# Optimization experiments

Measured on AMD Instinct MI355X. Metric: run time of the kernel, lower is better.

The kernel has to match this reference:

```python
import jax, jax.numpy as jnp
import numpy as np
import math

INNER = 96
EPS = 1e-8  # torch CosineSimilarity eps


def _proj(x, W1, W2):
    # nn.Linear(C,C,bias=False) -> ReLU -> nn.Linear(C,inner,bias=False)
    return jax.nn.relu(x @ W1) @ W2


def _cos(a, b):
    # torch CosineSimilarity(dim=-1): dot / (max(||a||,eps)*max(||b||,eps))
    num = jnp.sum(a * b, axis=-1)
    na = jnp.maximum(jnp.linalg.norm(a, axis=-1), EPS)
    nb = jnp.maximum(jnp.linalg.norm(b, axis=-1), EPS)
    return num / (na * nb)


def setup_inputs() -> dict:
    key = jax.random.key(0)
    ks = jax.random.split(key, 8)
    B, C, H, W = 128, 768, 7, 7
    sc1 = 1.0 / math.sqrt(C)
    inp = {
        "features_a": jax.random.normal(ks[0], (B, C, H, W), jnp.float32),
        "features_b": jax.random.normal(ks[1], (B, C, H, W), jnp.float32),
        "Wq1": jax.random.normal(ks[2], (C, C), jnp.float32) * sc1,
        "Wq2": jax.random.normal(ks[3], (C, INNER), jnp.float32) * sc1,
        "Wk1": jax.random.normal(ks[4], (C, C), jnp.float32) * sc1,
        "Wk2": jax.random.normal(ks[5], (C, INNER), jnp.float32) * sc1,
        "Wv1": jax.random.normal(ks[6], (C, C), jnp.float32) * sc1,
        "Wv2": jax.random.normal(ks[7], (C, INNER), jnp.float32) * sc1,
    }
    return inp


def reference(features_a, features_b, Wq1, Wq2, Wk1, Wk2, Wv1, Wv2):
    B, C = features_a.shape[0], features_a.shape[1]
    # [B, C, H, W] -> [B, S, C]
    fa = features_a.reshape(B, C, -1).transpose(0, 2, 1)
    fb = features_b.reshape(features_b.shape[0], C, -1).transpose(0, 2, 1)

    qa, ka, va = _proj(fa, Wq1, Wq2), _proj(fa, Wk1, Wk2), _proj(fa, Wv1, Wv2)
    qb, kb, vb = _proj(fb, Wq1, Wq2), _proj(fb, Wk1, Wk2), _proj(fb, Wv1, Wv2)

    scale = 1.0 / math.sqrt(INNER)

    # query_b vs key_a: [Bb, Ba, Sq, Sk]
    scores_ba = jnp.einsum('bqe,ake->baqk', qb, ka) * scale
    probs_ba = jax.nn.softmax(scores_ba, axis=-1)
    aligned_a = jnp.einsum('baqk,ake->baqe', probs_ba, va)  # [Bb, Ba, S, inner]

    # query_a vs key_b: [Bb, Ba, Sq, Sk]
    scores_ab = jnp.einsum('aqe,bke->baqk', qa, kb) * scale
    probs_ab = jax.nn.softmax(scores_ab, axis=-1)
    aligned_b = jnp.einsum('baqk,bke->baqe', probs_ab, vb)  # [Bb, Ba, S, inner]

    sim = _cos(va[None, :, :, :], aligned_b) + _cos(vb[:, None, :, :], aligned_a)
    return sim.mean(-1)  # [Bb, Ba]
```

## Files before the change

kernel.cpp:

```cpp
#include <hip/hip_runtime.h>
#include <hip/hip_bf16.h>
#include <math.h>

typedef __attribute__((ext_vector_type(8))) short bf16x8;
typedef __attribute__((ext_vector_type(4))) float f32x4;
typedef __attribute__((ext_vector_type(2))) float f32x2;

#define MROWS 12544
#define CDIM 768
#define INNER 96
#define S49 49
#define NSIDE 6272
#define SCALE 0.10206207261596577f
#define SCALE_EXP2 ((float)(0.10206207261596577 * 1.4426950408889634))

__device__ __forceinline__ unsigned short f2bf(float f) {
  union { float f; unsigned u; } v; v.f = f;
  unsigned u = v.u;
  return (unsigned short)((u + 0x7fffu + ((u >> 16) & 1u)) >> 16);
}
__device__ __forceinline__ float bf2f(unsigned short h) {
  union { unsigned u; float f; } v; v.u = ((unsigned)h) << 16;
  return v.f;
}
__device__ __forceinline__ unsigned pack_bf16_rn(float a, float b) {
  union { float f; unsigned u; } ua, ub; ua.f = a; ub.f = b;
  return __builtin_amdgcn_perm(ub.u + 0x8000u, ua.u + 0x8000u, 0x07060302u);
}

__device__ __forceinline__ void gld16(const unsigned short* g, unsigned short* l) {
  __builtin_amdgcn_global_load_lds(
      (const __attribute__((address_space(1))) unsigned int*)(g),
      (__attribute__((address_space(3))) unsigned int*)(l), 16, 0, 0);
}

__global__ __launch_bounds__(256) void prep_all(
    const float* __restrict__ fa, const float* __restrict__ fb,
    const float* __restrict__ w10, const float* __restrict__ w11,
    const float* __restrict__ w12, const float* __restrict__ w20,
    const float* __restrict__ w21, const float* __restrict__ w22,
    unsigned short* __restrict__ X,
    unsigned short* __restrict__ W1T, unsigned short* __restrict__ W2T,
    unsigned short* __restrict__ VtKpad) {
  const int t = threadIdx.x;
  int id = blockIdx.x;
  if (id < 3072) {
    __shared__ float T[64][50];
    const int z = id / 1536; id -= z * 1536;
    const int ct = id % 12, img = id / 12;
    const float* feat = z ? fb : fa;
    const float* src = feat + (size_t)img * (CDIM * S49) + (size_t)ct * 64 * S49;
    for (int idx = t; idx < 64 * S49; idx += 256) {
      int cc = idx / S49, s = idx - cc * S49;
      T[cc][s] = src[cc * S49 + s];
    }
    __syncthreads();
    unsigned short* dst = X + (size_t)(z * 128 + img) * S49 * CDIM + ct * 64;
    for (int idx = t; idx < S49 * 64; idx += 256) {
      int s = idx >> 6, cc = idx & 63;
      dst[(size_t)s * CDIM + cc] = f2bf(T[cc][s]);
    }
  } else if (id < 5016) {
    __shared__ float T[32][33];
    id -= 3072;
    const float* src;
    unsigned short* dst;
    int C, ctile, rtile;
    if (id < 1728) {
      int wdx = id / 576, tid = id - wdx * 576;
      ctile = tid % 24; rtile = tid / 24;
      src = wdx == 0 ? w10 : (wdx == 1 ? w11 : w12);
      dst = W1T + (size_t)wdx * CDIM * CDIM;
      C = CDIM;
    } else {
      id -= 1728;
      int wdx = id / 72, tid = id - wdx * 72;
      ctile = tid % 3; rtile = tid / 3;
      src = wdx == 0 ? w20 : (wdx == 1 ? w21 : w22);
      dst = W2T + (size_t)wdx * INNER * CDIM;
      C = INNER;
    }
    const int c0 = ctile * 32, r0 = rtile * 32;
    for (int idx = t; idx < 1024; idx += 256) {
      int rr = idx >> 5, cc = idx & 31;
      T[rr][cc] = src[(size_t)(r0 + rr) * C + c0 + cc];
    }
    __syncthreads();
    for (int idx = t; idx < 1024; idx += 256) {
      int rr = idx >> 5, cc = idx & 31;
      dst[(size_t)(c0 + rr) * CDIM + r0 + cc] = f2bf(T[cc][rr]);
    }
  } else {
    id -= 5016;
    ushort4* p4 = (ushort4*)VtKpad;
    const ushort4 z = make_ushort4(0, 0, 0, 0);
#pragma unroll
    for (int i = 0; i < 32; i++)
      p4[(size_t)id * 8192 + i * 256 + t] = z;
  }
}

#define BARR() do { __builtin_amdgcn_sched_barrier(0); \
  __builtin_amdgcn_s_barrier(); __builtin_amdgcn_sched_barrier(0); } while (0)
#define STG(src, dhalf) do { \
  gld16((src), (dhalf) + t8); \
  gld16((src) + 32, (dhalf) + t8 + 4096); } while (0)
#define MFMA_QUAD(QM, QN) do { \
  __builtin_amdgcn_s_setprio(1); \
  _Pragma("unroll") \
  for (int mi = 0; mi < 4; ++mi) { \
    _Pragma("unroll") \
    for (int ni = 0; ni < 2; ++ni) { \
      _Pragma("unroll") \
      for (int ks = 0; ks < 2; ++ks) \
        acc[(QM)*4+mi][(QN)*2+ni] = __builtin_amdgcn_mfma_f32_16x16x32_bf16( \
            Af[mi*2+ks], Bf[((QN)*2+ni)*2+ks], acc[(QM)*4+mi][(QN)*2+ni], \
            0, 0, 0); \
    } \
  } \
  __builtin_amdgcn_s_setprio(0); } while (0)

__global__ __launch_bounds__(512, 2) void gemm1_8p(
    const unsigned short* __restrict__ X,
    const unsigned short* __restrict__ W1T,
    unsigned short* __restrict__ H, int wbase, int hsel) {
  __shared__ __align__(16) unsigned short L[2][4][8192];
  const int t = threadIdx.x;
  const int lane = t & 63, w = t >> 6;
  const int lr = lane & 15, lq = lane >> 4;
  const int wm2 = w >> 2, wn4 = w & 3;
  const int gx = gridDim.x, gxy = gx * gridDim.y;
  const int nwg = gxy * gridDim.z;
  const int orig = blockIdx.x + gx * (blockIdx.y + gridDim.y * blockIdx.z);
  const int q8 = nwg >> 3, r8 = nwg & 7;
  const int xcd = orig & 7, rank = orig >> 3;
  const int logical = (xcd < r8 ? xcd * (q8 + 1) : r8 * (q8 + 1) + (xcd - r8) * q8) + rank;
  const int wdx_l = logical / gxy;
  const int rem = logical - wdx_l * gxy;
  const int M0 = (rem / gx) * 256, N0 = (rem % gx) * 256;
  const int wdx = wdx_l + wbase;
  const unsigned short* W1w = W1T + (size_t)wdx * CDIM * CDIM;
  unsigned short* Hw = H + (hsel ? (size_t)wdx * MROWS * CDIM : 0);

  const int rs = t >> 2;
  const int cs = ((t & 3) * 8) ^ (((rs >> 3) & 1) << 4);
  const int soff = rs * CDIM + cs;
  const unsigned short* pA0 = X + (size_t)M0 * CDIM + soff;
  const unsigned short* pA1 = pA0 + (size_t)128 * CDIM;
  const unsigned short* pB0 = W1w + (size_t)N0 * CDIM + soff;
  const unsigned short* pB1 = pB0 + (size_t)128 * CDIM;
  const int t8 = t * 8;

  const int rdbase = lr * 32 + ((lq * 8) ^ (((lr >> 3) & 1) << 4));
  const int bO = (wn4 & 1) * 2048;

  const f32x4 z4 = {0.f, 0.f, 0.f, 0.f};
  f32x4 acc[8][4];
#pragma unroll
  for (int i = 0; i < 8; ++i)
#pragma unroll
    for (int j = 0; j < 4; ++j) acc[i][j] = z4;
  bf16x8 Af[8], Bf[8];

  STG(pB0, &L[0][2][0]);
  STG(pA0, &L[0][0][0]);
  STG(pA1, &L[0][1][0]);
  STG(pB1, &L[0][3][0]);
  STG(pB0 + 64, &L[1][2][0]);
  STG(pA0 + 64, &L[1][0][0]);
  asm volatile("s_waitcnt vmcnt(4)" ::: "memory");
  BARR();

  for (int tau = 0; tau < 12; ++tau) {
    const int buf = tau & 1;
    const unsigned short* LA = &L[buf][wm2][0];
    const unsigned short* LB = &L[buf][2 + (wn4 >> 1)][0];
#pragma unroll
    for (int mf = 0; mf < 4; ++mf)
#pragma unroll
      for (int ks = 0; ks < 2; ++ks)
        Af[mf * 2 + ks] = *(const bf16x8*)(LA + ks * 4096 + mf * 512 + rdbase);
#pragma unroll
    for (int nf = 0; nf < 2; ++nf)
#pragma unroll
      for (int ks = 0; ks < 2; ++ks)
        Bf[nf * 2 + ks] = *(const bf16x8*)(LB + ks * 4096 + bO + nf * 512 + rdbase);
    if (tau + 1 < 12) STG(pA1 + (tau + 1) * 64, &L[(tau + 1) & 1][1][0]);
    BARR();
    MFMA_QUAD(0, 0);
    BARR();
#pragma unroll
    for (int nf = 2; nf < 4; ++nf)
#pragma unroll
      for (int ks = 0; ks < 2; ++ks)
        Bf[nf * 2 + ks] = *(const bf16x8*)(LB + ks * 4096 + bO + nf * 512 + rdbase);
    if (tau + 1 < 12) STG(pB1 + (tau + 1) * 64, &L[(tau + 1) & 1][3][0]);
    BARR();
    MFMA_QUAD(0, 1);
    BARR();
#pragma unroll
    for (int mf = 4; mf < 8; ++mf)
#pragma unroll
      for (int ks = 0; ks < 2; ++ks)
        Af[(mf - 4) * 2 + ks] = *(const bf16x8*)(LA + ks * 4096 + mf * 512 + rdbase);
    if (tau + 2 < 12) STG(pB0 + (tau + 2) * 64, &L[buf][2][0]);
    BARR();
    MFMA_QUAD(1, 0);
    BARR();
    if (tau + 2 < 12) STG(pA0 + (tau + 2) * 64, &L[buf][0][0]);
    if (tau < 10) {
      asm volatile("s_waitcnt vmcnt(4)" ::: "memory");
    } else if (tau == 10) {
      asm volatile("s_waitcnt vmcnt(0)" ::: "memory");
    }
    BARR();
    MFMA_QUAD(1, 1);
    BARR();
  }
#pragma unroll
  for (int mf = 0; mf < 8; ++mf)
#pragma unroll
    for (int nf = 0; nf < 4; ++nf)
#pragma unroll
      for (int r = 0; r < 4; ++r) {
        int m = M0 + wm2 * 128 + mf * 16 + lq * 4 + r;
        int n = N0 + wn4 * 64 + nf * 16 + lr;
        Hw[(size_t)m * CDIM + n] = f2bf(fmaxf(acc[mf][nf][r], 0.f));
      }
}

__global__ __launch_bounds__(512) void gemm2b5(const unsigned short* __restrict__ H,
                                               const unsigned short* __restrict__ W2T,
                                               unsigned short* __restrict__ QKV,
                                               unsigned short* __restrict__ Kpad,
                                               unsigned short* __restrict__ Vt,
                                               float* __restrict__ vnorm,
                                               int wbase, int hsel) {
  __shared__ __align__(16) unsigned short As[64 * 128];
  __shared__ __align__(16) unsigned short Bs[96 * 128];
  const int t = threadIdx.x;
  const int lane = t & 63, w = t >> 6;
  const int lr = lane & 15, lq = lane >> 4;
  const int wm = w & 3, we = w >> 2;
  const int m0 = blockIdx.x * 64;
  const int wdx = blockIdx.y + wbase;
  const unsigned short* Hw = H + (hsel ? (size_t)wdx * MROWS * CDIM : 0);
  const unsigned short* W2w = W2T + (size_t)wdx * INNER * CDIM;
  const f32x4 z4 = {0.f, 0.f, 0.f, 0.f};
  f32x4 acc[3] = {z4, z4, z4};

  for (int k0 = 0; k0 < CDIM; k0 += 128) {
    __syncthreads();
#pragma unroll
    for (int j = 0; j < 2; j++) {
      int l = t + j * 512;
      int row = l >> 4, ch = l & 15;
      gld16(Hw + (size_t)(m0 + row) * CDIM + k0 + (ch ^ (row & 7)) * 8, As + l * 8);
    }
#pragma unroll
    for (int j = 0; j < 3; j++) {
      int l = t + j * 512;
      int row = l >> 4, ch = l & 15;
      gld16(W2w + (size_t)row * CDIM + k0 + (ch ^ (row & 7)) * 8, Bs + l * 8);
    }
    __syncthreads();
#pragma unroll
    for (int kk = 0; kk < 4; kk++) {
      int ca = (kk * 4 + lq) ^ (lr & 7);
      bf16x8 a = *(const bf16x8*)(As + (wm * 16 + lr) * 128 + ca * 8);
#pragma unroll
      for (int et = 0; et < 3; et++) {
        bf16x8 b = *(const bf16x8*)(Bs + (we * 48 + et * 16 + lr) * 128 + ca * 8);
        acc[et] = __builtin_amdgcn_mfma_f32_16x16x32_bf16(a, b, acc[et], 0, 0, 0);
      }
    }
  }
  float nsq[4] = {0.f, 0.f, 0.f, 0.f};
#pragma unroll
  for (int et = 0; et < 3; et++)
#pragma unroll
    for (int r = 0; r < 4; r++) {
      int m = m0 + wm * 16 + lq * 4 + r;
      int e = we * 48 + et * 16 + lr;
      float v = acc[et][r];
      int img = m / 49, s = m - img * 49;
      if (wdx == 0) {
        QKV[(size_t)m * INNER + e] = f2bf(v * SCALE_EXP2);
      } else if (wdx == 1) {
        Kpad[(size_t)(img * 64 + s) * INNER + e] = f2bf(v);
      } else {
        QKV[(size_t)(2 * MROWS + m) * INNER + e] = f2bf(v);
        Vt[(size_t)img * (INNER * 64) + e * 64 + s] = f2bf(v);
        nsq[r] += v * v;
      }
    }
  if (wdx == 2) {
    __syncthreads();
    float (*nsqp)[64] = (float (*)[64])As;
#pragma unroll
    for (int r = 0; r < 4; r++) {
      float p = nsq[r];
      p += __shfl_xor(p, 1, 16);
      p += __shfl_xor(p, 2, 16);
      p += __shfl_xor(p, 4, 16);
      p += __shfl_xor(p, 8, 16);
      if (lr == 0) nsqp[we][wm * 16 + lq * 4 + r] = p;
    }
    __syncthreads();
    if (t < 64) vnorm[m0 + t] = sqrtf(nsqp[0][t] + nsqp[1][t]);
  }
}

__global__ __launch_bounds__(256) void attn13(const unsigned short* __restrict__ Qp,
                                              const unsigned short* __restrict__ Kpad,
                                              const unsigned short* __restrict__ V,
                                              const unsigned short* __restrict__ Vt,
                                              const float* __restrict__ vnorm,
                                              float* __restrict__ cosbuf) {
  __shared__ __align__(16) unsigned short Ks[64 * INNER];
  __shared__ __align__(16) unsigned short VtS[INNER * 64];
  __shared__ __align__(16) unsigned short Ps[4][32 * 64];

  const int t = threadIdx.x;
  const int lane = t & 63, w = t >> 6;
  const int lr = lane & 15, lq = lane >> 4;
  const f32x4 z4 = {0.f, 0.f, 0.f, 0.f};

  int bx = blockIdx.x;
  const int dir = bx / 784; bx -= dir * 784;
  const int chunk = bx >> 4, fg = bx & 15;
  const int r0 = chunk * 128;
  const int qbase = dir * NSIDE;

  int goK[3], goV[3], lo[3];
#pragma unroll
  for (int j = 0; j < 3; j++) {
    int l = (w * 3 + j) * 64 + lane;
    lo[j] = l * 8;
    int rK = l / 12, scK = l - rK * 12;
    int ccK = scK - ((rK >> 1) & 7); if (ccK < 0) ccK += 12;
    goK[j] = rK * INNER + ccK * 8;
    int rV = l >> 3, scV = l & 7;
    int ccV = (scV - (rV & 7)) & 7;
    goV[j] = rV * 64 + ccV * 8;
  }
  int rdK[3], rdV[2];
#pragma unroll
  for (int ks = 0; ks < 3; ks++) {
    int sc = (ks * 4 + lq + ((lr >> 1) & 7)) % 12;
    rdK[ks] = lr * INNER + sc * 8;
  }
#pragma unroll
  for (int ks = 0; ks < 2; ks++) {
    int sc = (ks * 4 + lq + (lr & 7)) & 7;
    rdV[ks] = lr * 64 + sc * 8;
  }

  bf16x8 qf[2][3];
#pragma unroll
  for (int qt = 0; qt < 2; qt++) {
    const int qrow = qbase + r0 + w * 32 + qt * 16 + lr;
#pragma unroll
    for (int ks = 0; ks < 3; ks++)
      qf[qt][ks] = *(const bf16x8*)(Qp + (size_t)qrow * INNER + ks * 32 + lq * 8);
  }
  f32x2 rv2[2][6][2];
  float invvn[2];
#pragma unroll
  for (int qt = 0; qt < 2; qt++) {
    const int qrow = qbase + r0 + w * 32 + qt * 16 + lr;
    invvn[qt] = 1.f / fmaxf(vnorm[qrow], 1e-8f);
#pragma unroll
    for (int et = 0; et < 6; et++) {
      ushort4 u = *(const ushort4*)(V + (size_t)qrow * INNER + et * 16 + lq * 4);
      rv2[qt][et][0] = (f32x2){bf2f(u.x), bf2f(u.y)};
      rv2[qt][et][1] = (f32x2){bf2f(u.z), bf2f(u.w)};
    }
  }

  unsigned short* Pw = &Ps[w][0];
  const int kimg0 = (dir == 0 ? 128 : 0) + fg * 8;
  {
    const unsigned short* kg = Kpad + (size_t)kimg0 * (64 * INNER);
#pragma unroll
    for (int j = 0; j < 3; j++) gld16(kg + goK[j], Ks + lo[j]);
  }
  for (int fi = 0; fi < 8; fi++) {
    const int f = fg * 8 + fi;
    __syncthreads();
    {
      const unsigned short* vg = Vt + (size_t)(kimg0 + fi) * (INNER * 64);
#pragma unroll
      for (int j = 0; j < 3; j++) gld16(vg + goV[j], VtS + lo[j]);
    }
    f32x4 s4[2][4] = {{z4, z4, z4, z4}, {z4, z4, z4, z4}};
    __builtin_amdgcn_s_setprio(1);
#pragma unroll
    for (int ks = 0; ks < 3; ks++) {
#pragma unroll
      for (int kt = 0; kt < 4; kt++) {
        bf16x8 a = *(const bf16x8*)(Ks + kt * (16 * INNER) + rdK[ks]);
        s4[0][kt] = __builtin_amdgcn_mfma_f32_16x16x32_bf16(a, qf[0][ks], s4[0][kt], 0, 0, 0);
        s4[1][kt] = __builtin_amdgcn_mfma_f32_16x16x32_bf16(a, qf[1][ks], s4[1][kt], 0, 0, 0);
      }
    }
    __builtin_amdgcn_s_setprio(0);
#pragma unroll
    for (int qt = 0; qt < 2; qt++)
#pragma unroll
      for (int kt = 0; kt < 4; kt++) {
        float e0 = __builtin_exp2f(s4[qt][kt][0]);
        float e1 = __builtin_exp2f(s4[qt][kt][1]);
        float e2 = __builtin_exp2f(s4[qt][kt][2]);
        float e3 = __builtin_exp2f(s4[qt][kt][3]);
        unsigned lopk, hipk;
        asm("v_cvt_pk_bf16_f32 %0, %1, %2" : "=v"(lopk) : "v"(e0), "v"(e1));
        asm("v_cvt_pk_bf16_f32 %0, %1, %2" : "=v"(hipk) : "v"(e2), "v"(e3));
        uint2 pk = make_uint2(lopk, hipk);
        int row = qt * 16 + lr;
        int ch = (2 * kt + (lq >> 1)) ^ (row & 7);
        *(uint2*)(Pw + row * 64 + ch * 8 + (lq & 1) * 4) = pk;
      }
    __syncthreads();
    if (fi < 7) {
      const unsigned short* kg = Kpad + (size_t)(kimg0 + fi + 1) * (64 * INNER);
#pragma unroll
      for (int j = 0; j < 3; j++) gld16(kg + goK[j], Ks + lo[j]);
    }
    f32x4 pv[2][6] = {{z4, z4, z4, z4, z4, z4}, {z4, z4, z4, z4, z4, z4}};
    __builtin_amdgcn_s_setprio(1);
#pragma unroll
    for (int ks = 0; ks < 2; ks++) {
      int row0 = 0 * 16 + lr, row1 = 1 * 16 + lr;
      int ch0 = ((ks * 4 + lq) ^ (row0 & 7));
      int ch1 = ((ks * 4 + lq) ^ (row1 & 7));
      bf16x8 b0 = *(const bf16x8*)(Pw + row0 * 64 + ch0 * 8);
      bf16x8 b1 = *(const bf16x8*)(Pw + row1 * 64 + ch1 * 8);
#pragma unroll
      for (int et = 0; et < 6; et++) {
        bf16x8 a = *(const bf16x8*)(VtS + et * (16 * 64) + rdV[ks]);
        pv[0][et] = __builtin_amdgcn_mfma_f32_16x16x32_bf16(a, b0, pv[0][et], 0, 0, 0);
        pv[1][et] = __builtin_amdgcn_mfma_f32_16x16x32_bf16(a, b1, pv[1][et], 0, 0, 0);
      }
    }
    __builtin_amdgcn_s_setprio(0);
#pragma unroll
    for (int qt = 0; qt < 2; qt++) {
      f32x2 dp = {0.f, 0.f}, np = {0.f, 0.f};
#pragma unroll
      for (int et = 0; et < 6; et++) {
        f32x2 al0 = __builtin_shufflevector(pv[qt][et], pv[qt][et], 0, 1);
        f32x2 al1 = __builtin_shufflevector(pv[qt][et], pv[qt][et], 2, 3);
        asm("v_pk_fma_f32 %0, %1, %2, %0" : "+v"(dp) : "v"(al0), "v"(rv2[qt][et][0]));
        asm("v_pk_fma_f32 %0, %1, %2, %0" : "+v"(np) : "v"(al0), "v"(al0));
        asm("v_pk_fma_f32 %0, %1, %2, %0" : "+v"(dp) : "v"(al1), "v"(rv2[qt][et][1]));
        asm("v_pk_fma_f32 %0, %1, %2, %0" : "+v"(np) : "v"(al1), "v"(al1));
      }
      float d = dp[0] + dp[1], nn = np[0] + np[1];
      d += __shfl_xor(d, 16, 64);  d += __shfl_xor(d, 32, 64);
      nn += __shfl_xor(nn, 16, 64); nn += __shfl_xor(nn, 32, 64);
      if (lane < 16) {
        float cv = d * __frsqrt_rn(fmaxf(nn, 1e-40f)) * invvn[qt];
        cosbuf[(size_t)(dir * 128 + f) * NSIDE + r0 + w * 32 + qt * 16 + lr] = cv;
      }
    }
  }
}

__global__ __launch_bounds__(256) void reduce_out(const float* __restrict__ cosbuf,
                                                  float* __restrict__ out) {
  const int t = threadIdx.x, lane = t & 63, wv = t >> 6;
  const int pair = blockIdx.x * 4 + wv;
  const int bb = pair >> 7, aa = pair & 127;
  float v = 0.f;
  if (lane < S49) {
    v  = cosbuf[(size_t)bb * NSIDE + aa * S49 + lane];
    v += cosbuf[(size_t)(128 + aa) * NSIDE + bb * S49 + lane];
  }
  for (int m = 1; m < 64; m <<= 1) v += __shfl_xor(v, m, 64);
  if (lane == 0) out[pair] = v * (1.f / 49.f);
}

extern "C" void kernel_launch(void* const* d_in, const int* in_sizes, int n_in,
                              void* d_out, int out_size, void* d_ws, size_t ws_size,
                              hipStream_t stream) {
  const float* fa  = (const float*)d_in[0];
  const float* fb  = (const float*)d_in[1];
  const float* W1[3] = {(const float*)d_in[2], (const float*)d_in[4], (const float*)d_in[6]};
  const float* W2[3] = {(const float*)d_in[3], (const float*)d_in[5], (const float*)d_in[7]};
  float* out = (float*)d_out;

  unsigned short* p = (unsigned short*)d_ws;
  unsigned short* Xbf = p;                 p += (size_t)MROWS * CDIM;
  unsigned short* W1T = p;                 p += (size_t)3 * CDIM * CDIM;
  unsigned short* W2T = p;                 p += (size_t)3 * INNER * CDIM;
  unsigned short* QKV = p;                 p += (size_t)3 * MROWS * INNER;
  unsigned short* Vt  = p;                 p += (size_t)256 * INNER * 64;
  unsigned short* Kpad = p;                p += (size_t)256 * 64 * INNER;
  float* vnorm = (float*)p;                p += (size_t)MROWS * 2;
  float* cosbuf = (float*)p;               p += (size_t)256 * NSIDE * 2;
  unsigned short* H = p;                   p += (size_t)3 * MROWS * CDIM;
  const size_t need_batched = (size_t)(p - (unsigned short*)d_ws) * 2;
  const int batched = ws_size >= need_batched;

  prep_all<<<dim3(5112), 256, 0, stream>>>(fa, fb, W1[0], W1[1], W1[2],
                                           W2[0], W2[1], W2[2],
                                           Xbf, W1T, W2T, Vt );
  if (batched) {
    gemm1_8p<<<dim3(CDIM / 256, MROWS / 256, 3), 512, 0, stream>>>(Xbf, W1T, H, 0, 1);
    gemm2b5<<<dim3(MROWS / 64, 3), 512, 0, stream>>>(H, W2T, QKV, Kpad, Vt, vnorm, 0, 1);
  } else {
    for (int wdx = 0; wdx < 3; wdx++) {
      gemm1_8p<<<dim3(CDIM / 256, MROWS / 256, 1), 512, 0, stream>>>(Xbf, W1T, H, wdx, 0);
      gemm2b5<<<dim3(MROWS / 64, 1), 512, 0, stream>>>(H, W2T, QKV, Kpad, Vt, vnorm, wdx, 0);
    }
  }
  attn13<<<dim3(2 * 784), 256, 0, stream>>>(
      QKV, Kpad, QKV + (size_t)2 * MROWS * INNER, Vt, vnorm, cosbuf);
  reduce_out<<<dim3(4096), 256, 0, stream>>>(cosbuf, out);
}
```

Baseline: 252.7 us.

## Fuse second projection GEMM into first GEMM epilogue with split-K partials

The first GEMM no longer writes the ReLU hidden activations H (3×12544×768 bf16) to global memory. Each 256×256 tile instead stores its ReLU'd bf16 tile into LDS and multiplies it by the matching 256-column slice of W2, writing fp32 partial outputs per N-slice. A small finalize kernel sums the three partials and does the scale, layout scatter and V-norm work that the old second GEMM did. The aim is to remove the large H round-trip and the separate gemm2 launch. The cost is extra fp32 partial traffic, an epilogue GEMM that reads W2 straight from global memory, and swapped warp roles inside the main loop.

Result: slower. 266.5 us (+5.5%).

```diff
diff --git a/kernel.cpp b/kernel.cpp
--- a/kernel.cpp
+++ b/kernel.cpp
@@ -105,42 +105,42 @@
 #define STG(src, dhalf) do { \
   gld16((src), (dhalf) + t8); \
   gld16((src) + 32, (dhalf) + t8 + 4096); } while (0)
-#define MFMA_QUAD(QM, QN) do { \
+#define MFMA_QUAD(QN, QM) do { \
   __builtin_amdgcn_s_setprio(1); \
   _Pragma("unroll") \
-  for (int mi = 0; mi < 4; ++mi) { \
+  for (int ni = 0; ni < 4; ++ni) { \
     _Pragma("unroll") \
-    for (int ni = 0; ni < 2; ++ni) { \
+    for (int mi = 0; mi < 2; ++mi) { \
       _Pragma("unroll") \
       for (int ks = 0; ks < 2; ++ks) \
-        acc[(QM)*4+mi][(QN)*2+ni] = __builtin_amdgcn_mfma_f32_16x16x32_bf16( \
-            Af[mi*2+ks], Bf[((QN)*2+ni)*2+ks], acc[(QM)*4+mi][(QN)*2+ni], \
-            0, 0, 0); \
+        acc[(QN)*4+ni][(QM)*2+mi] = __builtin_amdgcn_mfma_f32_16x16x32_bf16( \
+            Af[ni*2+ks], Bf[mi*2+ks], acc[(QN)*4+ni][(QM)*2+mi], 0, 0, 0); \
     } \
   } \
   __builtin_amdgcn_s_setprio(0); } while (0)
 
-__global__ __launch_bounds__(512, 2) void gemm1_8p(
+__global__ __launch_bounds__(512, 2) void gemm1f(
     const unsigned short* __restrict__ X,
     const unsigned short* __restrict__ W1T,
-    unsigned short* __restrict__ H, int wbase, int hsel) {
+    const unsigned short* __restrict__ W2T,
+    float* __restrict__ Opart) {
   __shared__ __align__(16) unsigned short L[2][4][8192];
+  unsigned short* Hl = &L[0][0][0];
   const int t = threadIdx.x;
   const int lane = t & 63, w = t >> 6;
   const int lr = lane & 15, lq = lane >> 4;
-  const int wm2 = w >> 2, wn4 = w & 3;
+  const int wn2 = w >> 2, wm4 = w & 3;
   const int gx = gridDim.x, gxy = gx * gridDim.y;
   const int nwg = gxy * gridDim.z;
   const int orig = blockIdx.x + gx * (blockIdx.y + gridDim.y * blockIdx.z);
   const int q8 = nwg >> 3, r8 = nwg & 7;
   const int xcd = orig & 7, rank = orig >> 3;
   const int logical = (xcd < r8 ? xcd * (q8 + 1) : r8 * (q8 + 1) + (xcd - r8) * q8) + rank;
-  const int wdx_l = logical / gxy;
-  const int rem = logical - wdx_l * gxy;
-  const int M0 = (rem / gx) * 256, N0 = (rem % gx) * 256;
-  const int wdx = wdx_l + wbase;
+  const int wdx = logical / gxy;
+  const int rem = logical - wdx * gxy;
+  const int M0 = (rem / gx) * 256, sl = rem % gx, N0 = sl * 256;
   const unsigned short* W1w = W1T + (size_t)wdx * CDIM * CDIM;
-  unsigned short* Hw = H + (hsel ? (size_t)wdx * MROWS * CDIM : 0);
+  const unsigned short* W2w = W2T + (size_t)wdx * INNER * CDIM;
 
   const int rs = t >> 2;
   const int cs = ((t & 3) * 8) ^ (((rs >> 3) & 1) << 4);
@@ -152,7 +152,7 @@
   const int t8 = t * 8;
 
   const int rdbase = lr * 32 + ((lq * 8) ^ (((lr >> 3) & 1) << 4));
-  const int bO = (wn4 & 1) * 2048;
+  const int aoff = (wm4 & 1) * 2048;
 
   const f32x4 z4 = {0.f, 0.f, 0.f, 0.f};
   f32x4 acc[8][4];
@@ -162,152 +162,178 @@
     for (int j = 0; j < 4; ++j) acc[i][j] = z4;
   bf16x8 Af[8], Bf[8];
 
-  STG(pB0, &L[0][2][0]);
   STG(pA0, &L[0][0][0]);
   STG(pA1, &L[0][1][0]);
+  STG(pB0, &L[0][2][0]);
   STG(pB1, &L[0][3][0]);
+  STG(pA0 + 64, &L[1][0][0]);
   STG(pB0 + 64, &L[1][2][0]);
-  STG(pA0 + 64, &L[1][0][0]);
   asm volatile("s_waitcnt vmcnt(4)" ::: "memory");
   BARR();
 
   for (int tau = 0; tau < 12; ++tau) {
     const int buf = tau & 1;
-    const unsigned short* LA = &L[buf][wm2][0];
-    const unsigned short* LB = &L[buf][2 + (wn4 >> 1)][0];
-#pragma unroll
-    for (int mf = 0; mf < 4; ++mf)
+    const unsigned short* LBa = &L[buf][2 + wn2][0];
+    const unsigned short* LAb = &L[buf][wm4 >> 1][0];
+#pragma unroll
+    for (int ni = 0; ni < 4; ++ni)
 #pragma unroll
       for (int ks = 0; ks < 2; ++ks)
-        Af[mf * 2 + ks] = *(const bf16x8*)(LA + ks * 4096 + mf * 512 + rdbase);
-#pragma unroll
-    for (int nf = 0; nf < 2; ++nf)
+        Af[ni * 2 + ks] = *(const bf16x8*)(LBa + ks * 4096 + ni * 512 + rdbase);
+#pragma unroll
+    for (int mi = 0; mi < 2; ++mi)
 #pragma unroll
       for (int ks = 0; ks < 2; ++ks)
-        Bf[nf * 2 + ks] = *(const bf16x8*)(LB + ks * 4096 + bO + nf * 512 + rdbase);
+        Bf[mi * 2 + ks] = *(const bf16x8*)(LAb + ks * 4096 + aoff + mi * 512 + rdbase);
     if (tau + 1 < 12) STG(pA1 + (tau + 1) * 64, &L[(tau + 1) & 1][1][0]);
     BARR();
     MFMA_QUAD(0, 0);
     BARR();
 #pragma unroll
-    for (int nf = 2; nf < 4; ++nf)
+    for (int mi = 0; mi < 2; ++mi)
 #pragma unroll
       for (int ks = 0; ks < 2; ++ks)
-        Bf[nf * 2 + ks] = *(const bf16x8*)(LB + ks * 4096 + bO + nf * 512 + rdbase);
+        Bf[4 + mi * 2 + ks] = *(const bf16x8*)(LAb + ks * 4096 + aoff + (2 + mi) * 512 + rdbase);
     if (tau + 1 < 12) STG(pB1 + (tau + 1) * 64, &L[(tau + 1) & 1][3][0]);
     BARR();
-    MFMA_QUAD(0, 1);
-    BARR();
-#pragma unroll
-    for (int mf = 4; mf < 8; ++mf)
+    {
+      __builtin_amdgcn_s_setprio(1);
+#pragma unroll
+      for (int ni = 0; ni < 4; ++ni)
+#pragma unroll
+        for (int mi = 0; mi < 2; ++mi)
+#pragma unroll
+          for (int ks = 0; ks < 2; ++ks)
+            acc[ni][2 + mi] = __builtin_amdgcn_mfma_f32_16x16x32_bf16(
+                Af[ni * 2 + ks], Bf[4 + mi * 2 + ks], acc[ni][2 + mi], 0, 0, 0);
+      __builtin_amdgcn_s_setprio(0);
+    }
+    BARR();
+#pragma unroll
+    for (int ni = 0; ni < 4; ++ni)
 #pragma unroll
       for (int ks = 0; ks < 2; ++ks)
-        Af[(mf - 4) * 2 + ks] = *(const bf16x8*)(LA + ks * 4096 + mf * 512 + rdbase);
+        Af[ni * 2 + ks] = *(const bf16x8*)(LBa + ks * 4096 + (4 + ni) * 512 + rdbase);
+    if (tau + 2 < 12) STG(pA0 + (tau + 2) * 64, &L[buf][0][0]);
+    BARR();
+    MFMA_QUAD(1, 0);
+    BARR();
     if (tau + 2 < 12) STG(pB0 + (tau + 2) * 64, &L[buf][2][0]);
-    BARR();
-    MFMA_QUAD(1, 0);
-    BARR();
-    if (tau + 2 < 12) STG(pA0 + (tau + 2) * 64, &L[buf][0][0]);
     if (tau < 10) {
       asm volatile("s_waitcnt vmcnt(4)" ::: "memory");
     } else if (tau == 10) {
       asm volatile("s_waitcnt vmcnt(0)" ::: "memory");
     }
     BARR();
-    MFMA_QUAD(1, 1);
-    BARR();
-  }
-#pragma unroll
-  for (int mf = 0; mf < 8; ++mf)
-#pragma unroll
-    for (int nf = 0; nf < 4; ++nf)
+    {
+      __builtin_amdgcn_s_setprio(1);
+#pragma unroll
+      for (int ni = 0; ni < 4; ++ni)
+#pragma unroll
+        for (int mi = 0; mi < 2; ++mi)
+#pragma unroll
+          for (int ks = 0; ks < 2; ++ks)
+            acc[4 + ni][2 + mi] = __builtin_amdgcn_mfma_f32_16x16x32_bf16(
+                Af[ni * 2 + ks], Bf[4 + mi * 2 + ks], acc[4 + ni][2 + mi], 0, 0, 0);
+      __builtin_amdgcn_s_setprio(0);
+    }
+    BARR();
+  }
+
+#pragma unroll
+  for (int nfr = 0; nfr < 8; ++nfr)
+#pragma unroll
+    for (int mfr = 0; mfr < 4; ++mfr) {
+      int m = wm4 * 64 + mfr * 16 + lr;
+      int nb = wn2 * 128 + nfr * 16 + lq * 4;
+      int c = (nb >> 3) ^ (m & 7);
+      f32x4 v = acc[nfr][mfr];
+      uint2 pk = make_uint2(pack_bf16_rn(fmaxf(v[0], 0.f), fmaxf(v[1], 0.f)),
+                            pack_bf16_rn(fmaxf(v[2], 0.f), fmaxf(v[3], 0.f)));
+      *(uint2*)(Hl + m * 256 + c * 8 + (lq & 1) * 4) = pk;
+    }
+  __syncthreads();
+
+  const int wmo = w >> 1, weo = w & 1;
+  f32x4 acc2[4][3];
+#pragma unroll
+  for (int i = 0; i < 4; ++i)
+#pragma unroll
+    for (int j = 0; j < 3; ++j) acc2[i][j] = z4;
+#pragma unroll
+  for (int ks = 0; ks < 8; ++ks) {
+    bf16x8 a[4], b[3];
+#pragma unroll
+    for (int mf = 0; mf < 4; ++mf) {
+      int m = wmo * 64 + mf * 16 + lr;
+      int cc = (ks * 4 + lq) ^ (m & 7);
+      a[mf] = *(const bf16x8*)(Hl + m * 256 + cc * 8);
+    }
+#pragma unroll
+    for (int ef = 0; ef < 3; ++ef) {
+      int e = weo * 48 + ef * 16 + lr;
+      b[ef] = *(const bf16x8*)(W2w + (size_t)e * CDIM + N0 + ks * 32 + lq * 8);
+    }
+#pragma unroll
+    for (int mf = 0; mf < 4; ++mf)
+#pragma unroll
+      for (int ef = 0; ef < 3; ++ef)
+        acc2[mf][ef] = __builtin_amdgcn_mfma_f32_16x16x32_bf16(a[mf], b[ef], acc2[mf][ef], 0, 0, 0);
+  }
+  float* Op = Opart + ((size_t)(sl * 3 + wdx) * MROWS + M0) * INNER;
+#pragma unroll
+  for (int mf = 0; mf < 4; ++mf)
+#pragma unroll
+    for (int ef = 0; ef < 3; ++ef)
 #pragma unroll
       for (int r = 0; r < 4; ++r) {
-        int m = M0 + wm2 * 128 + mf * 16 + lq * 4 + r;
-        int n = N0 + wn4 * 64 + nf * 16 + lr;
-        Hw[(size_t)m * CDIM + n] = f2bf(fmaxf(acc[mf][nf][r], 0.f));
+        int m = wmo * 64 + mf * 16 + lq * 4 + r;
+        int e = weo * 48 + ef * 16 + lr;
+        Op[(size_t)m * INNER + e] = acc2[mf][ef][r];
       }
 }
 
-__global__ __launch_bounds__(512) void gemm2b5(const unsigned short* __restrict__ H,
-                                               const unsigned short* __restrict__ W2T,
-                                               unsigned short* __restrict__ QKV,
-                                               unsigned short* __restrict__ Kpad,
-                                               unsigned short* __restrict__ Vt,
-                                               float* __restrict__ vnorm,
-                                               int wbase, int hsel) {
-  __shared__ __align__(16) unsigned short As[64 * 128];
-  __shared__ __align__(16) unsigned short Bs[96 * 128];
+__global__ __launch_bounds__(256) void finalize(const float* __restrict__ Opart,
+                                                unsigned short* __restrict__ QKV,
+                                                unsigned short* __restrict__ Kpad,
+                                                unsigned short* __restrict__ Vt,
+                                                float* __restrict__ vnorm) {
   const int t = threadIdx.x;
-  const int lane = t & 63, w = t >> 6;
-  const int lr = lane & 15, lq = lane >> 4;
-  const int wm = w & 3, we = w >> 2;
-  const int m0 = blockIdx.x * 64;
-  const int wdx = blockIdx.y + wbase;
-  const unsigned short* Hw = H + (hsel ? (size_t)wdx * MROWS * CDIM : 0);
-  const unsigned short* W2w = W2T + (size_t)wdx * INNER * CDIM;
-  const f32x4 z4 = {0.f, 0.f, 0.f, 0.f};
-  f32x4 acc[3] = {z4, z4, z4};
-
-  for (int k0 = 0; k0 < CDIM; k0 += 128) {
-    __syncthreads();
-#pragma unroll
-    for (int j = 0; j < 2; j++) {
-      int l = t + j * 512;
-      int row = l >> 4, ch = l & 15;
-      gld16(Hw + (size_t)(m0 + row) * CDIM + k0 + (ch ^ (row & 7)) * 8, As + l * 8);
-    }
-#pragma unroll
-    for (int j = 0; j < 3; j++) {
-      int l = t + j * 512;
-      int row = l >> 4, ch = l & 15;
-      gld16(W2w + (size_t)row * CDIM + k0 + (ch ^ (row & 7)) * 8, Bs + l * 8);
-    }
-    __syncthreads();
-#pragma unroll
-    for (int kk = 0; kk < 4; kk++) {
-      int ca = (kk * 4 + lq) ^ (lr & 7);
-      bf16x8 a = *(const bf16x8*)(As + (wm * 16 + lr) * 128 + ca * 8);
-#pragma unroll
-      for (int et = 0; et < 3; et++) {
-        bf16x8 b = *(const bf16x8*)(Bs + (we * 48 + et * 16 + lr) * 128 + ca * 8);
-        acc[et] = __builtin_amdgcn_mfma_f32_16x16x32_bf16(a, b, acc[et], 0, 0, 0);
-      }
-    }
-  }
-  float nsq[4] = {0.f, 0.f, 0.f, 0.f};
-#pragma unroll
-  for (int et = 0; et < 3; et++)
-#pragma unroll
-    for (int r = 0; r < 4; r++) {
-      int m = m0 + wm * 16 + lq * 4 + r;
-      int e = we * 48 + et * 16 + lr;
-      float v = acc[et][r];
-      int img = m / 49, s = m - img * 49;
-      if (wdx == 0) {
-        QKV[(size_t)m * INNER + e] = f2bf(v * SCALE_EXP2);
-      } else if (wdx == 1) {
-        Kpad[(size_t)(img * 64 + s) * INNER + e] = f2bf(v);
-      } else {
-        QKV[(size_t)(2 * MROWS + m) * INNER + e] = f2bf(v);
-        Vt[(size_t)img * (INNER * 64) + e * 64 + s] = f2bf(v);
-        nsq[r] += v * v;
-      }
-    }
+  const int m0 = blockIdx.x * 64, wdx = blockIdx.y;
+  const int ml = t >> 2, eq = t & 3;
+  const int m = m0 + ml;
+  const int e0 = eq * 24;
+  float o[24];
+#pragma unroll
+  for (int s = 0; s < 3; ++s) {
+    const float* src = Opart + ((size_t)(s * 3 + wdx) * MROWS + m) * INNER + e0;
+#pragma unroll
+    for (int j = 0; j < 6; ++j) {
+      float4 v = *(const float4*)(src + j * 4);
+      if (s == 0) { o[j*4] = v.x; o[j*4+1] = v.y; o[j*4+2] = v.z; o[j*4+3] = v.w; }
+      else { o[j*4] += v.x; o[j*4+1] += v.y; o[j*4+2] += v.z; o[j*4+3] += v.w; }
+    }
+  }
+  const int img = m / 49, s49 = m - img * 49;
+  float nsq = 0.f;
+#pragma unroll
+  for (int j = 0; j < 24; ++j) {
+    int e = e0 + j;
+    float v = o[j];
+    if (wdx == 0) {
+      QKV[(size_t)m * INNER + e] = f2bf(v * SCALE_EXP2);
+    } else if (wdx == 1) {
+      Kpad[(size_t)(img * 64 + s49) * INNER + e] = f2bf(v);
+    } else {
+      QKV[(size_t)(2 * MROWS + m) * INNER + e] = f2bf(v);
+      Vt[(size_t)img * (INNER * 64) + e * 64 + s49] = f2bf(v);
+      nsq += v * v;
+    }
+  }
   if (wdx == 2) {
-    __syncthreads();
-    float (*nsqp)[64] = (float (*)[64])As;
-#pragma unroll
-    for (int r = 0; r < 4; r++) {
-      float p = nsq[r];
-      p += __shfl_xor(p, 1, 16);
-      p += __shfl_xor(p, 2, 16);
-      p += __shfl_xor(p, 4, 16);
-      p += __shfl_xor(p, 8, 16);
-      if (lr == 0) nsqp[we][wm * 16 + lq * 4 + r] = p;
-    }
-    __syncthreads();
-    if (t < 64) vnorm[m0 + t] = sqrtf(nsqp[0][t] + nsqp[1][t]);
+    nsq += __shfl_xor(nsq, 1, 64);
+    nsq += __shfl_xor(nsq, 2, 64);
+    if (eq == 0) vnorm[m] = sqrtf(nsq);
   }
 }
 
@@ -499,22 +525,13 @@
   unsigned short* Kpad = p;                p += (size_t)256 * 64 * INNER;
   float* vnorm = (float*)p;                p += (size_t)MROWS * 2;
   float* cosbuf = (float*)p;               p += (size_t)256 * NSIDE * 2;
-  unsigned short* H = p;                   p += (size_t)3 * MROWS * CDIM;
-  const size_t need_batched = (size_t)(p - (unsigned short*)d_ws) * 2;
-  const int batched = ws_size >= need_batched;
+  float* Opart = (float*)p;                p += (size_t)9 * MROWS * INNER * 2;
 
   prep_all<<<dim3(5112), 256, 0, stream>>>(fa, fb, W1[0], W1[1], W1[2],
                                            W2[0], W2[1], W2[2],
                                            Xbf, W1T, W2T, Vt );
-  if (batched) {
-    gemm1_8p<<<dim3(CDIM / 256, MROWS / 256, 3), 512, 0, stream>>>(Xbf, W1T, H, 0, 1);
-    gemm2b5<<<dim3(MROWS / 64, 3), 512, 0, stream>>>(H, W2T, QKV, Kpad, Vt, vnorm, 0, 1);
-  } else {
-    for (int wdx = 0; wdx < 3; wdx++) {
-      gemm1_8p<<<dim3(CDIM / 256, MROWS / 256, 1), 512, 0, stream>>>(Xbf, W1T, H, wdx, 0);
-      gemm2b5<<<dim3(MROWS / 64, 1), 512, 0, stream>>>(H, W2T, QKV, Kpad, Vt, vnorm, wdx, 0);
-    }
-  }
+  gemm1f<<<dim3(CDIM / 256, MROWS / 256, 3), 512, 0, stream>>>(Xbf, W1T, W2T, Opart);
+  finalize<<<dim3(MROWS / 64, 3), 256, 0, stream>>>(Opart, QKV, Kpad, Vt, vnorm);
   attn13<<<dim3(2 * 784), 256, 0, stream>>>(
       QKV, Kpad, QKV + (size_t)2 * MROWS * INNER, Vt, vnorm, cosbuf);
   reduce_out<<<dim3(4096), 256, 0, stream>>>(cosbuf, out);
```
